# Kernel tuning notes

Hardware: AMD Instinct MI355X
Metric: run time of the kernel (lower is better)

The kernel has to match this reference:

```python
import jax, jax.numpy as jnp
import numpy as np

B, T, N, H = 16, 49, 24, 256
S = 0.05  # init scale (keeps sigmoids/tanh out of saturation for numeric testing)


def setup_inputs() -> dict:
    key = jax.random.key(0)
    ks = jax.random.split(key, 16)
    rn = lambda k, shp: (jax.random.normal(k, shp, dtype=jnp.float32) * S)
    return dict(
        h=rn(ks[0], (B, T, N, H)),
        c_h=rn(ks[1], (B, T, N, H)),
        p=rn(ks[2], (B, T, N, H)),
        g_t=rn(ks[3], (B, T, N, H)),
        c_g_t=rn(ks[4], (B, T, N, H)),
        g_s=rn(ks[5], (B, T, N, H)),
        c_g_s=rn(ks[6], (B, T, N, H)),
        # 9 h-gates stacked in order: i, lt, ft, rt, s, gt, gs, o, c
        U=rn(ks[7], (9, N, H, H)),
        Wt=rn(ks[8], (9, N, 3 * H, H)),
        Ws=rn(ks[9], (9, N, H, H)),
        Zt=rn(ks[10], (9, N, H, H)),
        Zs=rn(ks[11], (9, N, H, H)),
        b=rn(ks[12], (9, N, 1, H)),
        # 6 global gates stacked in order: gtf, gtg, gto, gsf, gsg, gso
        Wg=rn(ks[13], (6, N, H, H)),
        Zg=rn(ks[14], (6, N, H, H)),
        bg=rn(ks[15], (6, N, 1, H)),
        train=1,
    )


def _cell(h, c_h, p, g_t, c_g_t, g_s, c_g_s, U, Wt, Ws, Zt, Zs, b, Wg, Zg, bg):
    pad_t = jnp.zeros_like(h[:, :, :1, :])
    pad_s = jnp.zeros_like(h[:, :1, :, :])
    # spatial (bone) neighbours along axis 2
    h_t_before = jnp.concatenate([pad_t, h[:, :, :-1, :]], axis=2)
    h_t_after = jnp.concatenate([h[:, :, 1:, :], pad_t], axis=2)
    h_tba = jnp.concatenate([h_t_before, h, h_t_after], axis=3)  # [B,T,N,3H]
    c_t_before = jnp.concatenate([pad_t, c_h[:, :, :-1, :]], axis=2)
    c_t_after = jnp.concatenate([c_h[:, :, 1:, :], pad_t], axis=2)
    # temporal predecessor along axis 1
    h_s_before = jnp.concatenate([pad_s, h[:, :-1, :, :]], axis=1)
    c_s_before = jnp.concatenate([pad_s, c_h[:, :-1, :, :]], axis=1)

    # Faithful quirk of the source: f_ft gate uses Zslt (the lt gate's Zs) for its g_s term.
    Zs_eff = Zs.at[2].set(Zs[1])

    # All 9 gate preactivations in one fused batched-GEMM pass: [9,B,T,N,H]
    pre = (jnp.einsum('btnh,gnhk->gbtnk', p, U)
           + jnp.einsum('btnm,gnmk->gbtnk', h_tba, Wt)
           + jnp.einsum('btnh,gnhk->gbtnk', h_s_before, Ws)
           + jnp.einsum('btnh,gnhk->gbtnk', g_t, Zt)
           + jnp.einsum('btnh,gnhk->gbtnk', g_s, Zs_eff)
           + b[:, None, None, :, 0, :])
    i_n, f_lt, f_ft, f_rt, f_s, f_gt, f_gs, o_n = jax.nn.sigmoid(pre[:8])
    c_n = jnp.tanh(pre[8])

    c_h_new = (f_lt * c_t_before + f_ft * c_h + f_rt * c_t_after
               + f_s * c_s_before + f_gt * c_g_t + f_gs * c_g_s + i_n * c_n)
    h_new = o_n * jnp.tanh(c_h_new)

    def _global(x_g, c_g, Wg3, Zg3, bg3):
        pre_g = (jnp.einsum('btnh,gnhk->gbtnk', h_new, Wg3)
                 + jnp.einsum('btnh,gnhk->gbtnk', x_g, Zg3)
                 + bg3[:, None, None, :, 0, :])
        f_g = jax.nn.sigmoid(pre_g[0])
        cand = jnp.tanh(pre_g[1])
        o_g = jax.nn.sigmoid(pre_g[2])
        c_g_new = f_g * c_g + (1.0 - f_g) * cand
        return o_g * jnp.tanh(c_g_new), c_g_new

    g_t_new, c_g_t_new = _global(g_t, c_g_t, Wg[:3], Zg[:3], bg[:3])
    g_s_new, c_g_s_new = _global(g_s, c_g_s, Wg[3:], Zg[3:], bg[3:])
    return h_new, c_h_new, g_t_new, c_g_t_new, g_s_new, c_g_s_new


def reference(h, c_h, p, g_t, c_g_t, g_s, c_g_s, U, Wt, Ws, Zt, Zs, b, Wg, Zg, bg, train):
    # `train` is a flag unused by the cell's math (kept for signature fidelity)
    return _cell(h, c_h, p, g_t, c_g_t, g_s, c_g_s, U, Wt, Ws, Zt, Zs, b, Wg, Zg, bg)
```

## Files before the change

### kernel.cpp

```cpp
#include <hip/hip_runtime.h>
#include <hip/hip_bf16.h>

typedef unsigned short u16;
typedef u16 u16x8 __attribute__((ext_vector_type(8)));
typedef short s16x8 __attribute__((ext_vector_type(8)));
typedef float f32x4 __attribute__((ext_vector_type(4)));
typedef unsigned int u32;

#define NN 24
#define TT 49
#define MR 784
#define SZT 4816896

__device__ inline u16 f2b(float f){
    __hip_bfloat16 b = __float2bfloat16(f); u16 r; __builtin_memcpy(&r, &b, 2); return r;
}
__device__ inline float sig_(float x){ return 1.f / (1.f + __expf(-x)); }
__device__ inline float tanh_(float x){ float e = __expf(2.f * x); return (e - 1.f) / (e + 1.f); }

__device__ inline void gld16(const u16* g, u16* l){
    __builtin_amdgcn_global_load_lds(
        (const __attribute__((address_space(1))) unsigned int*)g,
        (__attribute__((address_space(3))) unsigned int*)l, 16, 0, 0);
}

#define BAR()      __builtin_amdgcn_s_barrier()
#define WAITVM(N)  asm volatile("s_waitcnt vmcnt(" #N ")" ::: "memory")
#define WAITVL(N)  asm volatile("s_waitcnt vmcnt(" #N ") lgkmcnt(0)" ::: "memory")

#define WT0_ELEMS ((size_t)216 * 256 * 1792)
#define WT1_ELEMS ((size_t)144 * 256 * 512)

__global__ __launch_bounds__(256) void prep_all(
    const float* __restrict__ U,  const float* __restrict__ Wt,
    const float* __restrict__ Ws, const float* __restrict__ Zt,
    const float* __restrict__ Zs, const float* __restrict__ Wg,
    const float* __restrict__ Zg,
    const float* __restrict__ p,  const float* __restrict__ h,
    const float* __restrict__ g_t, const float* __restrict__ g_s,
    u16* __restrict__ wt0, u16* __restrict__ wt1, u16* __restrict__ Abf)
{
    __shared__ u16 T[64][72];
    const int tid = threadIdx.x;
    const int lin = blockIdx.x;

    if (lin < 24192) {
        const int kt = lin % 28, ct = (lin / 28) % 4, z = lin / 112;
        const int n = z % NN, g = z / NN;
        const int k0 = kt * 64;
        const float* wbase;
        if (k0 < 256)       wbase = U  + (size_t)((g * NN + n) * 256 + k0)          * 256;
        else if (k0 < 1024) wbase = Wt + (size_t)((g * NN + n) * 768 + (k0 - 256))  * 256;
        else if (k0 < 1280) wbase = Ws + (size_t)((g * NN + n) * 256 + (k0 - 1024)) * 256;
        else if (k0 < 1536) wbase = Zt + (size_t)((g * NN + n) * 256 + (k0 - 1280)) * 256;
        else { const int g2 = (g == 2) ? 1 : g;
               wbase = Zs + (size_t)((g2 * NN + n) * 256 + (k0 - 1536)) * 256; }
        const int colg = ct * 64 + (tid & 15) * 4;
        #pragma unroll
        for (int it = 0; it < 4; ++it) {
            const int krl = (tid >> 4) + it * 16;
            const float4 v = *(const float4*)(wbase + (size_t)krl * 256 + colg);
            const int cl = (tid & 15) * 4;
            T[cl + 0][krl] = f2b(v.x); T[cl + 1][krl] = f2b(v.y);
            T[cl + 2][krl] = f2b(v.z); T[cl + 3][krl] = f2b(v.w);
        }
        __syncthreads();
        const int col_l = tid >> 2, ks = (tid & 3) * 16;
        const int ktile = 2 * kt + (ks >> 5);
        const int koff  = ks & 31;
        u16* dst = wt0 + (size_t)z * 458752 + (size_t)ktile * 8192
                       + (size_t)(ct * 64 + col_l) * 32 + koff;
        u16x8 w0, w1;
        #pragma unroll
        for (int j2 = 0; j2 < 8; ++j2) { w0[j2] = T[col_l][ks + j2]; w1[j2] = T[col_l][ks + 8 + j2]; }
        *(u16x8*)(dst) = w0; *(u16x8*)(dst + 8) = w1;
    } else if (lin < 28800) {
        const int l = lin - 24192;
        const int kt = l % 8, ct = (l / 8) % 4, z = l / 32;
        const int k0 = kt * 64;
        const float* wbase = (k0 < 256)
            ? Wg + (size_t)(z * 256 + k0) * 256
            : Zg + (size_t)(z * 256 + (k0 - 256)) * 256;
        const int colg = ct * 64 + (tid & 15) * 4;
        #pragma unroll
        for (int it = 0; it < 4; ++it) {
            const int krl = (tid >> 4) + it * 16;
            const float4 v = *(const float4*)(wbase + (size_t)krl * 256 + colg);
            const int cl = (tid & 15) * 4;
            T[cl + 0][krl] = f2b(v.x); T[cl + 1][krl] = f2b(v.y);
            T[cl + 2][krl] = f2b(v.z); T[cl + 3][krl] = f2b(v.w);
        }
        __syncthreads();
        const int col_l = tid >> 2, ks = (tid & 3) * 16;
        const int ktile = 2 * kt + (ks >> 5);
        const int koff  = ks & 31;
        u16* dst = wt1 + (size_t)z * 131072 + (size_t)ktile * 8192
                       + (size_t)(ct * 64 + col_l) * 32 + koff;
        u16x8 w0, w1;
        #pragma unroll
        for (int j2 = 0; j2 < 8; ++j2) { w0[j2] = T[col_l][ks + j2]; w1[j2] = T[col_l][ks + 8 + j2]; }
        *(u16x8*)(dst) = w0; *(u16x8*)(dst + 8) = w1;
    } else {
        const int l = lin - 28800;
        const int bx = l % 13, kt = (l / 13) % 56, n = l / 728;
        const int row = bx * 64 + (tid >> 2);
        if (row >= MR) return;
        const int c  = tid & 3;
        const int kg = kt * 32 + c * 8;
        const int seg = kg >> 8, koff = kg & 255;
        const int ec = (row * NN + n) * 256 + koff;
        const float* src = nullptr; bool valid = true;
        switch (seg) {
            case 0: src = p + ec; break;
            case 1: valid = (n > 0);          src = h + ec - 256; break;
            case 2: src = h + ec; break;
            case 3: valid = (n < NN - 1);     src = h + ec + 256; break;
            case 4: valid = (row % TT) != 0;  src = h + ec - NN * 256; break;
            case 5: src = g_t + ec; break;
            default: src = g_s + ec; break;
        }
        float4 lo = {0.f,0.f,0.f,0.f}, hi = lo;
        if (valid) { lo = *(const float4*)src; hi = *(const float4*)(src + 4); }
        u16x8 w;
        w[0] = f2b(lo.x); w[1] = f2b(lo.y); w[2] = f2b(lo.z); w[3] = f2b(lo.w);
        w[4] = f2b(hi.x); w[5] = f2b(hi.y); w[6] = f2b(hi.z); w[7] = f2b(hi.w);
        *(u16x8*)(Abf + ((size_t)(n * 56 + kt) * MR + row) * 32 + c * 8) = w;
    }
}

#define AB2 2048
#define BB2 18432

__global__ __launch_bounds__(256, 2) void fused_cell6(
    const float* __restrict__ c_h, const float* __restrict__ c_g_t,
    const float* __restrict__ c_g_s,
    const u16* __restrict__ Abf, const u16* __restrict__ WT0,
    const float* __restrict__ Bias,
    float* __restrict__ h_new, float* __restrict__ c_h_new)
{
    extern __shared__ u16 smem[];

    const int tid = threadIdx.x;
    const int lin = blockIdx.x;
    const int xcd = lin & 7, j = lin >> 3;
    const int mtile = j % 13;
    const int slab  = (j / 13) * 8 + xcd;
    const int ntile = slab & 3, n = slab >> 2;

    const int s_r = tid >> 2, s_c = tid & 3;
    const int wro = s_r * 32 + ((s_c ^ ((s_r >> 1) & 3)) << 3);

    const int wave = tid >> 6, lane = tid & 63;
    const int lrow = lane & 15, lci = lane >> 4;

    int aro[4];
    #pragma unroll
    for (int m = 0; m < 4; ++m) {
        const int row = m * 16 + lrow;
        aro[m] = row * 32 + ((lci ^ ((row >> 1) & 3)) << 3);
    }
    const int colr = wave * 16 + lrow;
    const int bro  = colr * 32 + ((lci ^ ((colr >> 1) & 3)) << 3);

    const u16* abase = Abf + ((size_t)(n * 56) * MR + mtile * 64) * 32 + wro;
    const u16* wbase = WT0 + (size_t)n * 458752 + (size_t)(ntile * 64) * 32 + wro;

    f32x4 acc[9][4];
    #pragma unroll
    for (int g = 0; g < 9; ++g)
        #pragma unroll
        for (int m = 0; m < 4; ++m) acc[g][m] = f32x4{0.f, 0.f, 0.f, 0.f};

    auto dma = [&](int kt, int buf) {
        gld16(abase + (size_t)kt * (MR * 32), &smem[buf * AB2 + tid * 8]);
        const u16* wb = wbase + (size_t)kt * 8192;
        u16* dst = &smem[2 * AB2 + buf * BB2 + tid * 8];
        #pragma unroll
        for (int g = 0; g < 9; ++g)
            gld16(wb + (size_t)g * 11010048, dst + g * 2048);
    };
    auto domfma = [&](int buf) {
        const u16* Asb = smem + buf * AB2;
        const u16* Bsb = smem + 2 * AB2 + buf * BB2;
        s16x8 af[4];
        #pragma unroll
        for (int m = 0; m < 4; ++m) af[m] = *(const s16x8*)(&Asb[aro[m]]);
        __builtin_amdgcn_s_setprio(1);
        #pragma unroll
        for (int g = 0; g < 9; ++g) {
            const s16x8 bf = *(const s16x8*)(&Bsb[g * 2048 + bro]);
            #pragma unroll
            for (int m = 0; m < 4; ++m)
                acc[g][m] = __builtin_amdgcn_mfma_f32_16x16x32_bf16(af[m], bf, acc[g][m], 0, 0, 0);
        }
        __builtin_amdgcn_s_setprio(0);
    };

    dma(0, 0);
    WAITVM(0); BAR();
    dma(1, 1);
    for (int kt = 0; kt < 54; kt += 2) {
        domfma(0);
        BAR();
        dma(kt + 2, 0);
        WAITVM(10); BAR();
        domfma(1);
        BAR();
        dma(kt + 3, 1);
        WAITVM(10); BAR();
    }
    domfma(0);
    BAR();
    WAITVM(0); BAR();
    domfma(1);

    const int col = ntile * 64 + wave * 16 + lrow;
    float bv[9];
    #pragma unroll
    for (int g = 0; g < 9; ++g) bv[g] = Bias[(g * NN + n) * 256 + col];

    #pragma unroll
    for (int m = 0; m < 4; ++m) {
        #pragma unroll
        for (int i = 0; i < 4; ++i) {
            const int row = mtile * 64 + m * 16 + (lane >> 4) * 4 + i;
            if (row < MR) {
                const size_t e = ((size_t)(row * NN + n)) * 256 + col;
                const float i_n  = sig_(acc[0][m][i] + bv[0]);
                const float f_lt = sig_(acc[1][m][i] + bv[1]);
                const float f_ft = sig_(acc[2][m][i] + bv[2]);
                const float f_rt = sig_(acc[3][m][i] + bv[3]);
                const float f_s  = sig_(acc[4][m][i] + bv[4]);
                const float f_gt = sig_(acc[5][m][i] + bv[5]);
                const float f_gs = sig_(acc[6][m][i] + bv[6]);
                const float o_n  = sig_(acc[7][m][i] + bv[7]);
                const float c_n  = tanh_(acc[8][m][i] + bv[8]);
                const float cb = (n > 0)      ? c_h[e - 256] : 0.f;
                const float ca = (n < NN - 1) ? c_h[e + 256] : 0.f;
                const float cs = (row % TT)   ? c_h[e - NN * 256] : 0.f;
                const float cn = f_lt * cb + f_ft * c_h[e] + f_rt * ca
                               + f_s * cs + f_gt * c_g_t[e] + f_gs * c_g_s[e]
                               + i_n * c_n;
                c_h_new[e] = cn;
                h_new[e]   = o_n * tanh_(cn);
            }
        }
    }
}

__global__ __launch_bounds__(256, 4) void fused_global5(
    const float* __restrict__ hn,   const float* __restrict__ g_t,
    const float* __restrict__ g_s,  const float* __restrict__ c_g_t,
    const float* __restrict__ c_g_s,
    const u16* __restrict__ WT1, const float* __restrict__ Bg,
    float* __restrict__ out2, float* __restrict__ out3,
    float* __restrict__ out4, float* __restrict__ out5)
{
    __shared__ u16 smem[2 * 2048 + 2 * 6144];

    const int tid = threadIdx.x;
    const int lin = blockIdx.x;
    const int xcd = lin & 7, j = lin >> 3;
    const int mtile = j % 13;
    const int slab  = (j / 13) * 8 + xcd;
    const int ntile = slab & 3;
    const int zz    = slab >> 2;
    const int n = zz % NN, grp = zz / NN;

    const float* xg = grp ? g_s : g_t;
    const float* cg = grp ? c_g_s : c_g_t;
    float* og  = grp ? out4 : out2;
    float* ocg = grp ? out5 : out3;

    const int s_r = tid >> 2, s_c = tid & 3;
    const int gr  = mtile * 64 + s_r;
    const bool mval = (gr < MR);
    const int ec = (gr * NN + n) * 256;

    const int wro = s_r * 32 + ((s_c ^ ((s_r >> 1) & 3)) << 3);

    const int wave = tid >> 6, lane = tid & 63;
    const int lrow = lane & 15, lci = lane >> 4;

    int aro[4];
    #pragma unroll
    for (int m = 0; m < 4; ++m) {
        const int row = m * 16 + lrow;
        aro[m] = row * 32 + ((lci ^ ((row >> 1) & 3)) << 3);
    }
    const int colr = wave * 16 + lrow;
    const int bro  = colr * 32 + ((lci ^ ((colr >> 1) & 3)) << 3);

    const u16* wbase = WT1 + (size_t)(grp * 3 * NN + n) * 131072
                           + (size_t)(ntile * 64) * 32 + wro;

    f32x4 acc[3][4];
    #pragma unroll
    for (int g = 0; g < 3; ++g)
        #pragma unroll
        for (int m = 0; m < 4; ++m) acc[g][m] = f32x4{0.f, 0.f, 0.f, 0.f};

    float4 aOlo, aOhi, aNlo, aNhi;

    auto loadA = [&](int kt, float4& lo, float4& hi) {
        const int K0 = kt * 32, koff = (K0 & 255) + s_c * 8;
        const float* src = ((K0 < 256) ? hn : xg) + ec + koff;
        lo = make_float4(0.f, 0.f, 0.f, 0.f); hi = lo;
        if (mval) { lo = *(const float4*)src; hi = *(const float4*)(src + 4); }
    };
    auto storeA = [&](int buf, const float4& lo, const float4& hi) {
        u16x8 aw;
        aw[0] = f2b(lo.x); aw[1] = f2b(lo.y); aw[2] = f2b(lo.z); aw[3] = f2b(lo.w);
        aw[4] = f2b(hi.x); aw[5] = f2b(hi.y); aw[6] = f2b(hi.z); aw[7] = f2b(hi.w);
        *(u16x8*)(&smem[buf * 2048 + wro]) = aw;
    };
    auto dmaB = [&](int kt, int buf) {
        const u16* wb = wbase + (size_t)kt * 8192;
        u16* dst = &smem[2 * 2048 + buf * 6144 + tid * 8];
        #pragma unroll
        for (int g = 0; g < 3; ++g)
            gld16(wb + (size_t)g * 3145728, dst + g * 2048);
    };
    auto domfma = [&](int buf) {
        const u16* Asb = smem + buf * 2048;
        const u16* Bsb = smem + 2 * 2048 + buf * 6144;
        s16x8 af[4];
        #pragma unroll
        for (int m = 0; m < 4; ++m) af[m] = *(const s16x8*)(&Asb[aro[m]]);
        __builtin_amdgcn_s_setprio(1);
        #pragma unroll
        for (int g = 0; g < 3; ++g) {
            const s16x8 bf = *(const s16x8*)(&Bsb[g * 2048 + bro]);
            #pragma unroll
            for (int m = 0; m < 4; ++m)
                acc[g][m] = __builtin_amdgcn_mfma_f32_16x16x32_bf16(af[m], bf, acc[g][m], 0, 0, 0);
        }
        __builtin_amdgcn_s_setprio(0);
    };

    loadA(0, aOlo, aOhi);
    dmaB(0, 0);
    storeA(0, aOlo, aOhi);
    loadA(1, aOlo, aOhi);
    dmaB(1, 1);
    WAITVL(5); BAR();
    for (int kt = 0; kt < 14; kt += 2) {
        domfma(0);
        BAR();
        loadA(kt + 2, aNlo, aNhi);
        dmaB(kt + 2, 0);
        storeA(1, aOlo, aOhi);
        WAITVL(5); BAR();
        domfma(1);
        BAR();
        loadA(kt + 3, aOlo, aOhi);
        dmaB(kt + 3, 1);
        storeA(0, aNlo, aNhi);
        WAITVL(5); BAR();
    }
    domfma(0);
    BAR();
    storeA(1, aOlo, aOhi);
    WAITVL(0); BAR();
    domfma(1);

    const int col = ntile * 64 + wave * 16 + lrow;
    float bv[3];
    #pragma unroll
    for (int g = 0; g < 3; ++g) bv[g] = Bg[((grp * 3 + g) * NN + n) * 256 + col];

    #pragma unroll
    for (int m = 0; m < 4; ++m) {
        #pragma unroll
        for (int i = 0; i < 4; ++i) {
            const int row = mtile * 64 + m * 16 + (lane >> 4) * 4 + i;
            if (row < MR) {
                const size_t e = ((size_t)(row * NN + n)) * 256 + col;
                const float f    = sig_(acc[0][m][i] + bv[0]);
                const float cand = tanh_(acc[1][m][i] + bv[1]);
                const float o    = sig_(acc[2][m][i] + bv[2]);
                const float cn = f * cg[e] + (1.f - f) * cand;
                ocg[e] = cn;
                og[e]  = o * tanh_(cn);
            }
        }
    }
}

extern "C" void kernel_launch(void* const* d_in, const int* in_sizes, int n_in,
                              void* d_out, int out_size, void* d_ws, size_t ws_size,
                              hipStream_t stream)
{
    const float* h     = (const float*)d_in[0];
    const float* c_h   = (const float*)d_in[1];
    const float* p     = (const float*)d_in[2];
    const float* g_t   = (const float*)d_in[3];
    const float* c_g_t = (const float*)d_in[4];
    const float* g_s   = (const float*)d_in[5];
    const float* c_g_s = (const float*)d_in[6];
    const float* U     = (const float*)d_in[7];
    const float* Wt    = (const float*)d_in[8];
    const float* Ws    = (const float*)d_in[9];
    const float* Zt    = (const float*)d_in[10];
    const float* Zs    = (const float*)d_in[11];
    const float* bb    = (const float*)d_in[12];
    const float* Wg    = (const float*)d_in[13];
    const float* Zg    = (const float*)d_in[14];
    const float* bg    = (const float*)d_in[15];

    float* out0 = (float*)d_out;
    float* out1 = out0 + (size_t)SZT;
    float* out2 = out1 + (size_t)SZT;
    float* out3 = out2 + (size_t)SZT;
    float* out4 = out3 + (size_t)SZT;
    float* out5 = out4 + (size_t)SZT;

    u16* wt0 = (u16*)d_ws;
    u16* wt1 = wt0 + WT0_ELEMS;
    u16* abf = wt1 + WT1_ELEMS;

    dim3 blk(256);
    prep_all<<<dim3(46272), blk, 0, stream>>>(U, Wt, Ws, Zt, Zs, Wg, Zg,
                                              p, h, g_t, g_s, wt0, wt1, abf);

    hipFuncSetAttribute((const void*)fused_cell6,
                        hipFuncAttributeMaxDynamicSharedMemorySize, 81920);
    fused_cell6<<<dim3(1248), blk, 81920, stream>>>(
        c_h, c_g_t, c_g_s, abf, wt0, bb, out0, out1);
    fused_global5<<<dim3(2496), blk, 0, stream>>>(
        out0, g_t, g_s, c_g_t, c_g_s, wt1, bg, out2, out3, out4, out5);
}
```

Baseline: 467.8 us.

## Fuse activation bf16 conversion into cell GEMM, drop staged A buffer

Removes the activation-staging part of the prep kernel that wrote a bf16 copy of the gathered [p, h neighbours, h_prev, g_t, g_s] matrix to global memory. The cell GEMM kernel now loads fp32 activations directly through registers, converts them to bf16 and writes them to LDS inside the double-buffered pipeline, while the weights still arrive by direct-to-LDS DMA. This saves one global write and read of the A operand. In exchange, each block reads fp32 activations, which is twice the bytes per element, and the 4 weight tiles share those activations, so each is re-read and re-converted. Register pressure also goes up under the 2-blocks-per-SIMD bound.

```diff
diff --git a/kernel.cpp b/kernel.cpp
--- a/kernel.cpp
+++ b/kernel.cpp
@@ -25,20 +25,17 @@
 }
 
 #define BAR()      __builtin_amdgcn_s_barrier()
-#define WAITVM(N)  asm volatile("s_waitcnt vmcnt(" #N ")" ::: "memory")
 #define WAITVL(N)  asm volatile("s_waitcnt vmcnt(" #N ") lgkmcnt(0)" ::: "memory")
 
 #define WT0_ELEMS ((size_t)216 * 256 * 1792)
 #define WT1_ELEMS ((size_t)144 * 256 * 512)
 
-__global__ __launch_bounds__(256) void prep_all(
+__global__ __launch_bounds__(256) void prep_w(
     const float* __restrict__ U,  const float* __restrict__ Wt,
     const float* __restrict__ Ws, const float* __restrict__ Zt,
     const float* __restrict__ Zs, const float* __restrict__ Wg,
     const float* __restrict__ Zg,
-    const float* __restrict__ p,  const float* __restrict__ h,
-    const float* __restrict__ g_t, const float* __restrict__ g_s,
-    u16* __restrict__ wt0, u16* __restrict__ wt1, u16* __restrict__ Abf)
+    u16* __restrict__ wt0, u16* __restrict__ wt1)
 {
     __shared__ u16 T[64][72];
     const int tid = threadIdx.x;
@@ -74,7 +71,7 @@
         #pragma unroll
         for (int j2 = 0; j2 < 8; ++j2) { w0[j2] = T[col_l][ks + j2]; w1[j2] = T[col_l][ks + 8 + j2]; }
         *(u16x8*)(dst) = w0; *(u16x8*)(dst + 8) = w1;
-    } else if (lin < 28800) {
+    } else {
         const int l = lin - 24192;
         const int kt = l % 8, ct = (l / 8) % 4, z = l / 32;
         const int k0 = kt * 64;
@@ -100,42 +97,18 @@
         #pragma unroll
         for (int j2 = 0; j2 < 8; ++j2) { w0[j2] = T[col_l][ks + j2]; w1[j2] = T[col_l][ks + 8 + j2]; }
         *(u16x8*)(dst) = w0; *(u16x8*)(dst + 8) = w1;
-    } else {
-        const int l = lin - 28800;
-        const int bx = l % 13, kt = (l / 13) % 56, n = l / 728;
-        const int row = bx * 64 + (tid >> 2);
-        if (row >= MR) return;
-        const int c  = tid & 3;
-        const int kg = kt * 32 + c * 8;
-        const int seg = kg >> 8, koff = kg & 255;
-        const int ec = (row * NN + n) * 256 + koff;
-        const float* src = nullptr; bool valid = true;
-        switch (seg) {
-            case 0: src = p + ec; break;
-            case 1: valid = (n > 0);          src = h + ec - 256; break;
-            case 2: src = h + ec; break;
-            case 3: valid = (n < NN - 1);     src = h + ec + 256; break;
-            case 4: valid = (row % TT) != 0;  src = h + ec - NN * 256; break;
-            case 5: src = g_t + ec; break;
-            default: src = g_s + ec; break;
-        }
-        float4 lo = {0.f,0.f,0.f,0.f}, hi = lo;
-        if (valid) { lo = *(const float4*)src; hi = *(const float4*)(src + 4); }
-        u16x8 w;
-        w[0] = f2b(lo.x); w[1] = f2b(lo.y); w[2] = f2b(lo.z); w[3] = f2b(lo.w);
-        w[4] = f2b(hi.x); w[5] = f2b(hi.y); w[6] = f2b(hi.z); w[7] = f2b(hi.w);
-        *(u16x8*)(Abf + ((size_t)(n * 56 + kt) * MR + row) * 32 + c * 8) = w;
     }
 }
 
 #define AB2 2048
 #define BB2 18432
 
-__global__ __launch_bounds__(256, 2) void fused_cell6(
-    const float* __restrict__ c_h, const float* __restrict__ c_g_t,
+__global__ __launch_bounds__(256, 2) void fused_cell7(
+    const float* __restrict__ p,   const float* __restrict__ h,
+    const float* __restrict__ c_h, const float* __restrict__ g_t,
+    const float* __restrict__ c_g_t, const float* __restrict__ g_s,
     const float* __restrict__ c_g_s,
-    const u16* __restrict__ Abf, const u16* __restrict__ WT0,
-    const float* __restrict__ Bias,
+    const u16* __restrict__ WT0, const float* __restrict__ Bias,
     float* __restrict__ h_new, float* __restrict__ c_h_new)
 {
     extern __shared__ u16 smem[];
@@ -148,6 +121,11 @@
     const int ntile = slab & 3, n = slab >> 2;
 
     const int s_r = tid >> 2, s_c = tid & 3;
+    const int gr  = mtile * 64 + s_r;
+    const bool mval = (gr < MR);
+    const int ec = (gr * NN + n) * 256;
+    const bool vnb = (n > 0), vna = (n < NN - 1), vtp = (gr % TT) != 0;
+
     const int wro = s_r * 32 + ((s_c ^ ((s_r >> 1) & 3)) << 3);
 
     const int wave = tid >> 6, lane = tid & 63;
@@ -162,7 +140,6 @@
     const int colr = wave * 16 + lrow;
     const int bro  = colr * 32 + ((lci ^ ((colr >> 1) & 3)) << 3);
 
-    const u16* abase = Abf + ((size_t)(n * 56) * MR + mtile * 64) * 32 + wro;
     const u16* wbase = WT0 + (size_t)n * 458752 + (size_t)(ntile * 64) * 32 + wro;
 
     f32x4 acc[9][4];
@@ -171,8 +148,30 @@
         #pragma unroll
         for (int m = 0; m < 4; ++m) acc[g][m] = f32x4{0.f, 0.f, 0.f, 0.f};
 
-    auto dma = [&](int kt, int buf) {
-        gld16(abase + (size_t)kt * (MR * 32), &smem[buf * AB2 + tid * 8]);
+    float4 aOlo, aOhi, aNlo, aNhi;
+
+    auto loadA = [&](int kt, float4& lo, float4& hi) {
+        const int K0 = kt * 32, seg = K0 >> 8, koff = (K0 & 255) + s_c * 8;
+        const float* src = nullptr; bool valid = mval;
+        switch (seg) {
+            case 0: src = p + ec + koff; break;
+            case 1: valid &= vnb; src = h + ec - 256 + koff; break;
+            case 2: src = h + ec + koff; break;
+            case 3: valid &= vna; src = h + ec + 256 + koff; break;
+            case 4: valid &= vtp; src = h + ec - NN * 256 + koff; break;
+            case 5: src = g_t + ec + koff; break;
+            default: src = g_s + ec + koff; break;
+        }
+        lo = make_float4(0.f, 0.f, 0.f, 0.f); hi = lo;
+        if (valid) { lo = *(const float4*)src; hi = *(const float4*)(src + 4); }
+    };
+    auto storeA = [&](int buf, const float4& lo, const float4& hi) {
+        u16x8 aw;
+        aw[0] = f2b(lo.x); aw[1] = f2b(lo.y); aw[2] = f2b(lo.z); aw[3] = f2b(lo.w);
+        aw[4] = f2b(hi.x); aw[5] = f2b(hi.y); aw[6] = f2b(hi.z); aw[7] = f2b(hi.w);
+        *(u16x8*)(&smem[buf * AB2 + wro]) = aw;
+    };
+    auto dmaB = [&](int kt, int buf) {
         const u16* wb = wbase + (size_t)kt * 8192;
         u16* dst = &smem[2 * AB2 + buf * BB2 + tid * 8];
         #pragma unroll
@@ -196,22 +195,31 @@
         __builtin_amdgcn_s_setprio(0);
     };
 
-    dma(0, 0);
-    WAITVM(0); BAR();
-    dma(1, 1);
+    loadA(0, aOlo, aOhi);
+    dmaB(0, 0);
+    storeA(0, aOlo, aOhi);
+    loadA(1, aOlo, aOhi);
+    dmaB(1, 1);
+    WAITVL(11); BAR();
+
     for (int kt = 0; kt < 54; kt += 2) {
         domfma(0);
         BAR();
-        dma(kt + 2, 0);
-        WAITVM(10); BAR();
+        loadA(kt + 2, aNlo, aNhi);
+        dmaB(kt + 2, 0);
+        storeA(1, aOlo, aOhi);
+        WAITVL(11); BAR();
         domfma(1);
         BAR();
-        dma(kt + 3, 1);
-        WAITVM(10); BAR();
+        loadA(kt + 3, aOlo, aOhi);
+        dmaB(kt + 3, 1);
+        storeA(0, aNlo, aNhi);
+        WAITVL(11); BAR();
     }
     domfma(0);
     BAR();
-    WAITVM(0); BAR();
+    storeA(1, aOlo, aOhi);
+    WAITVL(0); BAR();
     domfma(1);
 
     const int col = ntile * 64 + wave * 16 + lrow;
@@ -417,16 +425,14 @@
 
     u16* wt0 = (u16*)d_ws;
     u16* wt1 = wt0 + WT0_ELEMS;
-    u16* abf = wt1 + WT1_ELEMS;
 
     dim3 blk(256);
-    prep_all<<<dim3(46272), blk, 0, stream>>>(U, Wt, Ws, Zt, Zs, Wg, Zg,
-                                              p, h, g_t, g_s, wt0, wt1, abf);
-
-    hipFuncSetAttribute((const void*)fused_cell6,
+    prep_w<<<dim3(28800), blk, 0, stream>>>(U, Wt, Ws, Zt, Zs, Wg, Zg, wt0, wt1);
+
+    hipFuncSetAttribute((const void*)fused_cell7,
                         hipFuncAttributeMaxDynamicSharedMemorySize, 81920);
-    fused_cell6<<<dim3(1248), blk, 81920, stream>>>(
-        c_h, c_g_t, c_g_s, abf, wt0, bb, out0, out1);
+    fused_cell7<<<dim3(1248), blk, 81920, stream>>>(
+        p, h, c_h, g_t, c_g_t, g_s, c_g_s, wt0, bb, out0, out1);
     fused_global5<<<dim3(2496), blk, 0, stream>>>(
         out0, g_t, g_s, c_g_t, c_g_s, wt1, bg, out2, out3, out4, out5);
 }
```

Result: slower. 512.8 us (+9.6%).

## Enlarge cell GEMM tile to 128 rows with 8-wave blocks sharing weight tiles

Applied to the files above, without the earlier changes.

The fused cell kernel moves from 256-thread blocks covering 64 rows to 512-thread blocks covering 128 rows, with two row halves sharing each weight tile loaded into LDS. This halves weight traffic per output row and cuts the grid from 1248 to 672 blocks. Weight DMA is redistributed unevenly across waves (5 or 4 loads each), with per-wave vmcnt waits before the barrier. The cost is more LDS per block, one block per CU, and more padded rows in the last M tile (784 is not a multiple of 128).

```diff
diff --git a/kernel.cpp b/kernel.cpp
--- a/kernel.cpp
+++ b/kernel.cpp
@@ -128,10 +128,10 @@
     }
 }
 
-#define AB2 2048
-#define BB2 18432
-
-__global__ __launch_bounds__(256, 2) void fused_cell6(
+#define AB8 4096
+#define BB8 18432
+
+__global__ __launch_bounds__(512, 1) void fused_cell8(
     const float* __restrict__ c_h, const float* __restrict__ c_g_t,
     const float* __restrict__ c_g_s,
     const u16* __restrict__ Abf, const u16* __restrict__ WT0,
@@ -143,28 +143,44 @@
     const int tid = threadIdx.x;
     const int lin = blockIdx.x;
     const int xcd = lin & 7, j = lin >> 3;
-    const int mtile = j % 13;
-    const int slab  = (j / 13) * 8 + xcd;
+    const int mtile = j % 7;
+    const int slab  = (j / 7) * 8 + xcd;
     const int ntile = slab & 3, n = slab >> 2;
 
-    const int s_r = tid >> 2, s_c = tid & 3;
-    const int wro = s_r * 32 + ((s_c ^ ((s_r >> 1) & 3)) << 3);
-
     const int wave = tid >> 6, lane = tid & 63;
+    const int rh = wave >> 2, cq = wave & 3;
     const int lrow = lane & 15, lci = lane >> 4;
 
+    const int rloc = wave * 16 + (lane >> 2);
+    const int rglb = mtile * 128 + rloc;
+    const int rsrc = (rglb < MR) ? rglb : (MR - 1);
+    const int ach  = (lane & 3) ^ ((rloc >> 1) & 3);
+    const u16* aSrc = Abf + ((size_t)(n * 56) * MR + rsrc) * 32 + ach * 8;
+    const int aDst = wave * 512 + lane * 8;
+
+    const int g0 = (wave < 4) ? wave * 5 : 20 + (wave - 4) * 4;
+    const int ng = (wave < 4) ? 5 : 4;
+    const u16* bSrc[5]; int bDst[5];
+    #pragma unroll
+    for (int i = 0; i < 5; ++i) {
+        const int G = g0 + ((i < ng) ? i : 0);
+        const int g = G >> 2, q = G & 3;
+        const int c = q * 16 + (lane >> 2);
+        const int ch = (lane & 3) ^ ((c >> 1) & 3);
+        bSrc[i] = WT0 + (size_t)n * 458752 + (size_t)g * 11010048
+                + (size_t)(ntile * 64 + c) * 32 + ch * 8;
+        bDst[i] = g * 2048 + q * 512 + lane * 8;
+    }
+
     int aro[4];
     #pragma unroll
     for (int m = 0; m < 4; ++m) {
-        const int row = m * 16 + lrow;
+        const int row = rh * 64 + m * 16 + lrow;
         aro[m] = row * 32 + ((lci ^ ((row >> 1) & 3)) << 3);
     }
-    const int colr = wave * 16 + lrow;
+    const int colr = cq * 16 + lrow;
     const int bro  = colr * 32 + ((lci ^ ((colr >> 1) & 3)) << 3);
 
-    const u16* abase = Abf + ((size_t)(n * 56) * MR + mtile * 64) * 32 + wro;
-    const u16* wbase = WT0 + (size_t)n * 458752 + (size_t)(ntile * 64) * 32 + wro;
-
     f32x4 acc[9][4];
     #pragma unroll
     for (int g = 0; g < 9; ++g)
@@ -172,16 +188,20 @@
         for (int m = 0; m < 4; ++m) acc[g][m] = f32x4{0.f, 0.f, 0.f, 0.f};
 
     auto dma = [&](int kt, int buf) {
-        gld16(abase + (size_t)kt * (MR * 32), &smem[buf * AB2 + tid * 8]);
-        const u16* wb = wbase + (size_t)kt * 8192;
-        u16* dst = &smem[2 * AB2 + buf * BB2 + tid * 8];
-        #pragma unroll
-        for (int g = 0; g < 9; ++g)
-            gld16(wb + (size_t)g * 11010048, dst + g * 2048);
+        gld16(aSrc + (size_t)kt * (MR * 32), &smem[buf * AB8 + aDst]);
+        const size_t ko = (size_t)kt * 8192;
+        u16* bBase = &smem[2 * AB8 + buf * BB8];
+        #pragma unroll
+        for (int i = 0; i < 5; ++i)
+            if (i < ng) gld16(bSrc[i] + ko, bBase + bDst[i]);
+    };
+    auto publish = [&]() {
+        if (wave < 4) { WAITVM(6); } else { WAITVM(5); }
+        BAR();
     };
     auto domfma = [&](int buf) {
-        const u16* Asb = smem + buf * AB2;
-        const u16* Bsb = smem + 2 * AB2 + buf * BB2;
+        const u16* Asb = smem + buf * AB8;
+        const u16* Bsb = smem + 2 * AB8 + buf * BB8;
         s16x8 af[4];
         #pragma unroll
         for (int m = 0; m < 4; ++m) af[m] = *(const s16x8*)(&Asb[aro[m]]);
@@ -203,18 +223,18 @@
         domfma(0);
         BAR();
         dma(kt + 2, 0);
-        WAITVM(10); BAR();
+        publish();
         domfma(1);
         BAR();
         dma(kt + 3, 1);
-        WAITVM(10); BAR();
+        publish();
     }
     domfma(0);
     BAR();
     WAITVM(0); BAR();
     domfma(1);
 
-    const int col = ntile * 64 + wave * 16 + lrow;
+    const int col = ntile * 64 + cq * 16 + lrow;
     float bv[9];
     #pragma unroll
     for (int g = 0; g < 9; ++g) bv[g] = Bias[(g * NN + n) * 256 + col];
@@ -223,7 +243,7 @@
     for (int m = 0; m < 4; ++m) {
         #pragma unroll
         for (int i = 0; i < 4; ++i) {
-            const int row = mtile * 64 + m * 16 + (lane >> 4) * 4 + i;
+            const int row = mtile * 128 + rh * 64 + m * 16 + (lane >> 4) * 4 + i;
             if (row < MR) {
                 const size_t e = ((size_t)(row * NN + n)) * 256 + col;
                 const float i_n  = sig_(acc[0][m][i] + bv[0]);
@@ -423,9 +443,9 @@
     prep_all<<<dim3(46272), blk, 0, stream>>>(U, Wt, Ws, Zt, Zs, Wg, Zg,
                                               p, h, g_t, g_s, wt0, wt1, abf);
 
-    hipFuncSetAttribute((const void*)fused_cell6,
-                        hipFuncAttributeMaxDynamicSharedMemorySize, 81920);
-    fused_cell6<<<dim3(1248), blk, 81920, stream>>>(
+    hipFuncSetAttribute((const void*)fused_cell8,
+                        hipFuncAttributeMaxDynamicSharedMemorySize, 90112);
+    fused_cell8<<<dim3(672), dim3(512), 90112, stream>>>(
         c_h, c_g_t, c_g_s, abf, wt0, bb, out0, out1);
     fused_global5<<<dim3(2496), blk, 0, stream>>>(
         out0, g_t, g_s, c_g_t, c_g_s, wt1, bg, out2, out3, out4, out5);
```

Result: no change. 470.4 us (+0.5%).
